# Performance work log

Measured on AMD Instinct MI355X. Metric: run time of the kernel, lower is better.

Reference implementation:

```python
import itertools
import jax, jax.numpy as jnp
import numpy as np

# ---- static config (matches init_kwargs) ----
FRAME_H, FRAME_W = 480, 640
RES = 5               # map_resolution (cm/cell)
Z_RES = 5
MAP_SIZE_CM = 4800 // 2   # after global_downscaling
VR = 100              # vision_range
HFOV = 79.0
DU = 1                # du_scale
CAT_THR, EXP_THR, MAP_THR = 5.0, 1.0, 1.0
NSEM = 16
MAX_H = int(360 / Z_RES)    # 72
MIN_H = int(-80 / Z_RES)    # -16
AGENT_H_CM = 0.88 * 100.0
XC = (FRAME_W - 1.0) / 2.0
ZC = (FRAME_H - 1.0) / 2.0
FOCAL = (FRAME_W / 2.0) / np.tan(np.deg2rad(HFOV / 2.0))
VFOV = np.arctan(FRAME_H / 2.0 / FOCAL)
MIN_VISION = AGENT_H_CM / np.tan(VFOV)
SHIFT_X = VR * RES // 2     # shift_loc[0]; rotation angle is 0 -> identity
DEG = 57.29577951308232


def splat_feat_nd(grid_dims, feat, coords):
    # feat: (B,F,N); coords: (B,3,N) in [-1,1]; trilinear scatter-add splat.
    B, Fc, N = feat.shape
    pos_dim, wts_dim = [], []
    for d in range(3):
        g = grid_dims[d]
        pos = coords[:, d, :] * (g / 2.0) + g / 2.0
        pd, wd = [], []
        for ix in (0, 1):
            p = jnp.floor(pos) + ix
            safe = ((p > 0) & (p < g)).astype(feat.dtype)
            wd.append((1.0 - jnp.abs(pos - p)) * safe)
            pd.append(p * safe)
        pos_dim.append(pd)
        wts_dim.append(wd)
    gflat = jnp.zeros((B, Fc, grid_dims[0] * grid_dims[1] * grid_dims[2]), feat.dtype)
    scatter = jax.vmap(lambda g, i, u: g.at[:, i].add(u))
    for ix_d in itertools.product((0, 1), (0, 1), (0, 1)):
        index = jnp.zeros((B, N), feat.dtype)
        wts = jnp.ones((B, N), feat.dtype)
        for d in range(3):
            index = index * grid_dims[d] + pos_dim[d][ix_d[d]]
            wts = wts * wts_dim[d][ix_d[d]]
        upd = feat * wts[:, None, :]
        gflat = jnp.round(scatter(gflat, index.astype(jnp.int32), upd))  # torch rounds after each pass
    return gflat.reshape(B, Fc, grid_dims[0], grid_dims[1], grid_dims[2])


def affine_grid(theta, H, W):
    # torch F.affine_grid, align_corners=False (default)
    xs = (2.0 * jnp.arange(W) + 1.0) / W - 1.0
    ys = (2.0 * jnp.arange(H) + 1.0) / H - 1.0
    X, Y = jnp.meshgrid(xs, ys, indexing='xy')          # (H,W)
    base = jnp.stack([X, Y, jnp.ones_like(X)], -1)      # (H,W,3)
    return jnp.einsum('bij,hwj->bhwi', theta, base)     # (B,H,W,2)


def grid_sample(img, grid):
    # bilinear, zeros padding, align_corners=True (as in forward)
    B, C, H, W = img.shape
    x = (grid[..., 0] + 1.0) * 0.5 * (W - 1)
    y = (grid[..., 1] + 1.0) * 0.5 * (H - 1)
    x0 = jnp.floor(x)
    y0 = jnp.floor(y)

    def gather(ix, iy):
        valid = ((ix >= 0) & (ix <= W - 1) & (iy >= 0) & (iy <= H - 1)).astype(img.dtype)
        ic = jnp.clip(ix, 0, W - 1).astype(jnp.int32)
        jc = jnp.clip(iy, 0, H - 1).astype(jnp.int32)
        v = jax.vmap(lambda im, jj, ii: im[:, jj, ii])(img, jc, ic)  # (B,C,Ho,Wo)
        return v * valid[:, None]

    wx1 = x - x0
    wx0 = 1.0 - wx1
    wy1 = y - y0
    wy0 = 1.0 - wy1
    return (gather(x0, y0) * (wx0 * wy0)[:, None]
            + gather(x0 + 1, y0) * (wx1 * wy0)[:, None]
            + gather(x0, y0 + 1) * (wx0 * wy1)[:, None]
            + gather(x0 + 1, y0 + 1) * (wx1 * wy1)[:, None])


def reference(obs, pose_obs, maps_last, poses_last, agent_heights):
    bs, c, h, w = obs.shape
    depth = obs[:, 3]
    # ---- point cloud from depth (camera frame) ----
    Y = depth[:, ::DU, ::DU]
    gx = jnp.arange(w, dtype=obs.dtype)[::DU]            # pixel x (width)
    gz = jnp.arange(h - 1, -1, -1, dtype=obs.dtype)[::DU]  # flipped pixel z (height)
    X = (gx[None, None, :] - XC) * Y / FOCAL
    Z = (gz[None, :, None] - ZC) * Y / FOCAL
    Z = Z + agent_heights * 100.0   # camera elevation 0 -> rotation is identity
    X = X + SHIFT_X                 # shift_loc angle pi/2 -> rotation is identity
    # ---- normalize to [-1,1] voxel coords ----
    Xc = ((X / RES) - VR // 2.0) / VR * 2.0
    Yc = ((Y / RES) - VR // 2.0) / VR * 2.0
    Zc = ((Z / Z_RES) - (MAX_H + MIN_H) // 2.0) / (MAX_H - MIN_H) * 2.0
    coords = jnp.stack([Xc, Yc, Zc], axis=1).reshape(bs, 3, -1)   # (B,3,N)
    # ---- per-point features: [occupancy=1, avg-pooled semantics] ----
    hs, ws = h // DU, w // DU
    sem = obs[:, 4:].reshape(bs, c - 4, hs, DU, ws, DU).mean(axis=(3, 5))
    feat = jnp.concatenate([jnp.ones((bs, 1, hs * ws), obs.dtype),
                            sem.reshape(bs, c - 4, hs * ws)], axis=1)
    # ---- splat into voxel grid, then height-axis projections ----
    voxels = splat_feat_nd((VR, VR, MAX_H - MIN_H), feat, coords).swapaxes(2, 3)
    min_z = int(35 / Z_RES - MIN_H)               # 23
    max_z = int((AGENT_H_CM + 1) / Z_RES - MIN_H)  # 33
    floor_z = int(-35 / Z_RES - MIN_H)             # 9
    agent_height_proj = voxels[..., min_z:max_z].sum(-1)
    all_height_proj = voxels.sum(-1)
    mv_std = int(MIN_VISION // Z_RES)
    around_floor = voxels[..., :min_z].sum(-1)
    under_floor = (voxels[..., floor_z:min_z].sum(-1) == 0.0).astype(obs.dtype) * around_floor
    # near-field floor heuristic from last depth row
    depth_row = depth[:, -1, :]
    re_depth = jnp.where(depth_row < 3000.0, depth_row, jnp.asarray(MIN_VISION, obs.dtype))
    count = (re_depth - MIN_VISION - 60.0 > 0).sum(axis=1)
    mask = count > (w / 4.0)
    c1, c2 = (VR - 6) // 2, (VR + 6) // 2
    patch = under_floor[:, 0, mv_std, c1:c2]
    under_floor = under_floor.at[:, 0, mv_std, c1:c2].set(jnp.where(mask[:, None], 1.0, patch))
    fp_map_pred = jnp.clip((agent_height_proj[:, 0:1] + under_floor[:, 0:1]) / MAP_THR, 0.0, 1.0)
    fp_exp_pred = jnp.clip(all_height_proj[:, 0:1] / EXP_THR, 0.0, 1.0)
    # ---- paste into egocentric local map frame ----
    M = MAP_SIZE_CM // RES   # 480
    x1 = M // 2 - VR // 2
    x2 = x1 + VR
    y1 = M // 2
    y2 = y1 + VR
    agent_view = jnp.zeros((bs, c, M, M), obs.dtype)
    agent_view = agent_view.at[:, 0:1, y1:y2, x1:x2].set(fp_map_pred)
    agent_view = agent_view.at[:, 1:2, y1:y2, x1:x2].set(fp_exp_pred)
    agent_view = agent_view.at[:, 4:, y1:y2, x1:x2].set(
        jnp.clip(agent_height_proj[:, 1:] / CAT_THR, 0.0, 1.0))
    # ---- dead-reckoning pose update ----
    th = poses_last[:, 2] / DEG
    ny = poses_last[:, 1] + pose_obs[:, 0] * jnp.sin(th) + pose_obs[:, 1] * jnp.cos(th)
    nx = poses_last[:, 0] + pose_obs[:, 0] * jnp.cos(th) - pose_obs[:, 1] * jnp.sin(th)
    nt = poses_last[:, 2] + pose_obs[:, 2] * DEG
    nt = jnp.fmod(nt - 180.0, 360.0) + 180.0
    nt = jnp.fmod(nt + 180.0, 360.0) - 180.0
    current_poses = jnp.stack([nx, ny, nt], axis=1)
    # ---- spatial transform (rotate then translate) into allocentric map ----
    half = M // 2
    stx = -(nx * 100.0 / RES - half) / half
    sty = -(ny * 100.0 / RES - half) / half
    t = (90.0 - nt) * np.pi / 180.0
    cos_t, sin_t = jnp.cos(t), jnp.sin(t)
    zeros, ones = jnp.zeros_like(cos_t), jnp.ones_like(cos_t)
    theta1 = jnp.stack([jnp.stack([cos_t, -sin_t, zeros], 1),
                        jnp.stack([sin_t, cos_t, zeros], 1)], 1)
    theta2 = jnp.stack([jnp.stack([ones, zeros, stx], 1),
                        jnp.stack([zeros, ones, sty], 1)], 1)
    rotated = grid_sample(agent_view, affine_grid(theta1, M, M))
    translated = grid_sample(rotated, affine_grid(theta2, M, M))
    map_pred = jnp.maximum(maps_last, translated)
    # pose_pred aliases the in-place-updated poses_last in torch == current_poses
    return fp_map_pred, map_pred, current_poses, current_poses


def setup_inputs():
    key = jax.random.key(0)
    k1, k2, k3, k4, k5, k6 = jax.random.split(key, 6)
    bs, c, h, w = 8, 4 + NSEM, FRAME_H, FRAME_W
    obs = jax.random.uniform(k1, (bs, c, h, w), jnp.float32)            # RGB/sem in [0,1]
    depth = jax.random.uniform(k2, (bs, h, w), jnp.float32) * 480.0 + 20.0  # cm
    obs = obs.at[:, 3].set(depth)
    pose_obs = jax.random.normal(k3, (bs, 3), jnp.float32) * jnp.array([0.1, 0.1, 0.05], jnp.float32)
    maps_last = jax.random.uniform(k4, (bs, c, 480, 480), jnp.float32)
    xy = jax.random.uniform(k5, (bs, 2), jnp.float32) * 4.0 + 10.0      # meters, near map center
    ang = jax.random.uniform(k6, (bs, 1), jnp.float32) * 360.0 - 180.0
    poses_last = jnp.concatenate([xy, ang], axis=1)
    agent_heights = jnp.full((bs, 1, 1), 0.88, jnp.float32)
    return {"obs": obs, "pose_obs": pose_obs, "maps_last": maps_last,
            "poses_last": poses_last, "agent_heights": agent_heights}
```

## Files before the change

kernel.cpp:

```cpp
#include <hip/hip_runtime.h>
#include <math.h>

#pragma clang fp contract(off)

#define BS 8
#define CCH 20
#define IMH 480
#define IMW 640
#define HW (IMH*IMW)
#define VRX 100
#define NZ 88
#define NSEMC 16
#define CROP0 124
#define CROPN 232
#define NROTC 18
#define NBINS 880000
#define NBINS2 80000
#define SEMCAP 890000u

__global__ void posemask_kernel(const float* __restrict__ pose_obs,
                                const float* __restrict__ poses_last,
                                const float* __restrict__ obs,
                                float* __restrict__ outp1, float* __restrict__ outp2,
                                float* __restrict__ posebuf, float MINVF) {
#pragma clang fp contract(off)
  int b = blockIdx.x;
  int t = threadIdx.x;
  if (t == 0) {
    const float DEGF = (float)57.29577951308232;
    float th = poses_last[b*3+2] / DEGF;
    float sn = sinf(th), cs = cosf(th);
    float ny = poses_last[b*3+1] + pose_obs[b*3+0]*sn + pose_obs[b*3+1]*cs;
    float nx = poses_last[b*3+0] + pose_obs[b*3+0]*cs - pose_obs[b*3+1]*sn;
    float nt = poses_last[b*3+2] + pose_obs[b*3+2]*DEGF;
    nt = fmodf(nt - 180.0f, 360.0f) + 180.0f;
    nt = fmodf(nt + 180.0f, 360.0f) - 180.0f;
    outp1[b*3+0] = nx; outp1[b*3+1] = ny; outp1[b*3+2] = nt;
    outp2[b*3+0] = nx; outp2[b*3+1] = ny; outp2[b*3+2] = nt;
    float tt = (90.0f - nt) * (float)M_PI / 180.0f;
    float* pb = posebuf + b*8;
    pb[0] = cosf(tt);
    pb[1] = sinf(tt);
    pb[2] = -((nx*100.0f/5.0f - 240.0f)/240.0f);
    pb[3] = -((ny*100.0f/5.0f - 240.0f)/240.0f);
  }
  const float* row = obs + (size_t)b*CCH*HW + 3*(size_t)HW + 479*IMW;
  int cnt = 0;
  for (int col = t; col < IMW; col += 256) {
    float d = row[col];
    float re = (d < 3000.0f) ? d : MINVF;
    float v = re - MINVF;
    v = v - 60.0f;
    if (v > 0.0f) cnt++;
  }
  __shared__ int sh[256];
  sh[t] = cnt;
  __syncthreads();
  for (int s = 128; s > 0; s >>= 1) {
    if (t < s) sh[t] += sh[t + s];
    __syncthreads();
  }
  if (t == 0) posebuf[b*8+4] = (sh[0] > 160) ? 1.0f : 0.0f;
}

__device__ __forceinline__ void transform_pix(int r, int col, float Yd, float ah100,
                                              float FOCALF,
                                              float& pos0, float& pos1, float& pos2) {
#pragma clang fp contract(off)
  float X = ((float)col - 319.5f) * Yd / FOCALF;
  X = X + 250.0f;
  float Z = ((float)(479 - r) - 239.5f) * Yd / FOCALF;
  Z = Z + ah100;
  float Xc = (X/5.0f - 50.0f)/100.0f*2.0f;
  float Yc = (Yd/5.0f - 50.0f)/100.0f*2.0f;
  float Zc = (Z/5.0f - 28.0f)/88.0f*2.0f;
  pos0 = Xc*50.0f + 50.0f;
  pos1 = Yc*50.0f + 50.0f;
  pos2 = Zc*44.0f + 44.0f;
}

__device__ __forceinline__ int bin_key(int b, float pos0, float pos1, float pos2) {
  float f0 = floorf(pos0), f1 = floorf(pos1), f2 = floorf(pos2);
  if (!(f0 >= 0.0f && f0 <= 99.0f && f1 >= 0.0f && f1 <= 99.0f &&
        f2 >= 0.0f && f2 <= 87.0f)) return -1;
  int xi = (int)f0, yi = (int)f1, zi = (int)f2;
  return ((b*100 + yi)*100 + xi)*11 + (zi >> 3);
}

__global__ void bin_count_kernel(const float* __restrict__ obs,
                                 const float* __restrict__ agent_h,
                                 unsigned* __restrict__ cnt, unsigned* __restrict__ cnt2,
                                 float FOCALF) {
#pragma clang fp contract(off)
  int tid = blockIdx.x*256 + threadIdx.x;
#pragma unroll
  for (int u = 0; u < 4; u++) {
    int p = tid + u*614400;
    int b = p / HW;
    int pix = p - b*HW;
    int r = pix / IMW, col = pix - r*IMW;
    float Yd = obs[(size_t)b*CCH*HW + 3*(size_t)HW + pix];
    float ah100 = agent_h[b]*100.0f;
    float pos0, pos1, pos2;
    transform_pix(r, col, Yd, ah100, FOCALF, pos0, pos1, pos2);
    int key = bin_key(b, pos0, pos1, pos2);
    if (key >= 0) {
      atomicAdd(&cnt[key], 1u);
      int zi = (int)floorf(pos2);
      if (zi >= 22 && zi <= 32) atomicAdd(&cnt2[key/11], 1u);
    }
  }
}

__device__ __forceinline__ void scan1_body(const unsigned* __restrict__ cnt,
                                           unsigned* __restrict__ offs,
                                           unsigned* __restrict__ bsum,
                                           int n, int blk, unsigned* sh) {
  int t = threadIdx.x;
  int base = blk*1024 + t*4;
  unsigned v[4];
  unsigned s = 0;
#pragma unroll
  for (int i = 0; i < 4; i++) {
    unsigned c = (base + i < n) ? cnt[base + i] : 0u;
    v[i] = s; s += c;
  }
  sh[t] = s;
  __syncthreads();
  for (int off = 1; off < 256; off <<= 1) {
    unsigned add = (t >= off) ? sh[t - off] : 0u;
    __syncthreads();
    sh[t] += add;
    __syncthreads();
  }
  unsigned texcl = sh[t] - s;
#pragma unroll
  for (int i = 0; i < 4; i++)
    if (base + i < n) offs[base + i] = texcl + v[i];
  if (t == 255) bsum[blk] = sh[255];
}

__global__ void scan1m_kernel(const unsigned* __restrict__ cnt, unsigned* __restrict__ offs,
                              unsigned* __restrict__ bsum,
                              const unsigned* __restrict__ cnt2, unsigned* __restrict__ offs2,
                              unsigned* __restrict__ bsum2) {
  __shared__ unsigned sh[256];
  int blk = blockIdx.x;
  if (blk < 860) scan1_body(cnt, offs, bsum, NBINS, blk, sh);
  else           scan1_body(cnt2, offs2, bsum2, NBINS2, blk - 860, sh);
}

__global__ void scan2m_kernel(unsigned* __restrict__ bsum, unsigned* __restrict__ bsum2) {
  __shared__ unsigned sh[1024];
  unsigned* arr = (blockIdx.x == 0) ? bsum : bsum2;
  int nb = (blockIdx.x == 0) ? 860 : 79;
  int t = threadIdx.x;
  unsigned v = (t < nb) ? arr[t] : 0u;
  sh[t] = v;
  __syncthreads();
  for (int off = 1; off < 1024; off <<= 1) {
    unsigned add = (t >= off) ? sh[t - off] : 0u;
    __syncthreads();
    sh[t] += add;
    __syncthreads();
  }
  if (t < nb) arr[t] = sh[t] - v;
}

__global__ void scan3m_kernel(unsigned* __restrict__ offs, const unsigned* __restrict__ bsum,
                              unsigned* __restrict__ cursor,
                              unsigned* __restrict__ offs2, const unsigned* __restrict__ bsum2,
                              unsigned* __restrict__ cursor2) {
  int blk = blockIdx.x;
  if (blk < 3438) {
    int i = blk*256 + threadIdx.x;
    if (i >= NBINS) return;
    unsigned o = offs[i] + bsum[i >> 10];
    offs[i] = o;
    cursor[i] = o;
  } else {
    int i = (blk - 3438)*256 + threadIdx.x;
    if (i >= NBINS2) return;
    unsigned o = offs2[i] + bsum2[i >> 10];
    offs2[i] = o;
    cursor2[i] = o;
  }
}

__global__ void place_kernel(const float* __restrict__ obs,
                             const float* __restrict__ agent_h,
                             unsigned* __restrict__ cursor,
                             float4* __restrict__ records, float FOCALF) {
#pragma clang fp contract(off)
  int tid = blockIdx.x*256 + threadIdx.x;
#pragma unroll
  for (int u = 0; u < 2; u++) {
    int p = tid + u*1228800;
    int b = p / HW;
    int pix = p - b*HW;
    int r = pix / IMW, col = pix - r*IMW;
    float Yd = obs[(size_t)b*CCH*HW + 3*(size_t)HW + pix];
    float ah100 = agent_h[b]*100.0f;
    float pos0, pos1, pos2;
    transform_pix(r, col, Yd, ah100, FOCALF, pos0, pos1, pos2);
    int key = bin_key(b, pos0, pos1, pos2);
    if (key >= 0) {
      unsigned idx = atomicAdd(&cursor[key], 1u);
      float4 rec;
      rec.x = pos0; rec.y = pos1; rec.z = pos2; rec.w = 0.0f;
      records[idx] = rec;
    }
  }
}

__global__ void __launch_bounds__(256) gatherS_cm_kernel(
    const float4* __restrict__ records, const unsigned* __restrict__ offs,
    const unsigned* __restrict__ cursor, float* __restrict__ colbuf) {
#pragma clang fp contract(off)
  __shared__ float S[256*9];
  __shared__ float red[32][8][4];
  int t = threadIdx.x;
  int k = t & 7, cw = t >> 3;
  int iz = k & 1, ix = (k >> 1) & 1, iy = (k >> 2) & 1;
  int col = blockIdx.x*32 + cw;
  int cx = col % 100, cy = (col/100) % 100;
  bool cellvalid = (cx+ix >= 1) && (cx+ix <= 99) && (cy+iy >= 1) && (cy+iy <= 99);
  float fx = (float)ix, fy = (float)iy, fz = (float)iz;
  float* Sl = &S[t*9];
#pragma unroll
  for (int i = 0; i < 8; i++) Sl[i] = 0.0f;
  float pall = 0.f, pahp = 0.f, par = 0.f, pmid = 0.f;
  int colkey = col*11;
  for (int oct = 0; oct < 11; oct++) {
    unsigned s = offs[colkey + oct], e = cursor[colkey + oct];
    for (unsigned ri = s; ri < e; ri++) {
      float4 rec = records[ri];
      float f0 = floorf(rec.x), f1 = floorf(rec.y), f2 = floorf(rec.z);
      float wx = 1.0f - fabsf(rec.x - (f0 + fx));
      float wy = 1.0f - fabsf(rec.y - (f1 + fy));
      float wz = 1.0f - fabsf(rec.z - (f2 + fz));
      float w = wx*wy;
      w = w*wz;
      int z8 = ((int)f2) & 7;
      Sl[z8] += w;
    }
    int zbase = oct*8;
#pragma unroll
    for (int z8 = 0; z8 < 8; z8++) {
      float a = Sl[z8];
      Sl[z8] = 0.0f;
      int tz = zbase + z8 + iz;
      if (a != 0.0f && tz >= 1 && tz <= 87) {
        float rv = rintf(a);
        pall += rv;
        if (tz < 23) { par += rv; if (tz >= 9) pmid += rv; }
        else if (tz < 33) pahp += rv;
      }
    }
  }
  if (!cellvalid) { pall = 0.f; pahp = 0.f; par = 0.f; pmid = 0.f; }
  red[cw][k][0] = pall;
  red[cw][k][1] = pahp;
  red[cw][k][2] = par;
  red[cw][k][3] = pmid;
  __syncthreads();
  for (int e2 = t; e2 < 512; e2 += 256) {
    int cw2 = e2 >> 4, rem = e2 & 15, c = rem >> 2, p = rem & 3;
    int colw = blockIdx.x*32 + cw2;
    colbuf[colw*16 + rem] = red[cw2][2*c][p] + red[cw2][2*c + 1][p];
  }
}

__global__ void combine_kernel(const float* __restrict__ colbuf,
                               const float* __restrict__ posebuf,
                               float* __restrict__ out0, float* __restrict__ fpexp) {
#pragma clang fp contract(off)
  int tid = blockIdx.x*256 + threadIdx.x;
  if (tid >= 80000) return;
  int b = tid / 10000;
  int yx = tid - b*10000;
  int ty = yx / 100, tx = yx - (yx/100)*100;
  float all = 0.f, ahp = 0.f, ar = 0.f, mid = 0.f;
#pragma unroll
  for (int c = 0; c < 4; c++) {
    int iy = c >> 1, ix = c & 1;
    int cy = ty - iy, cx = tx - ix;
    if (cy < 0 || cx < 0) continue;
    const float* cb = &colbuf[((b*10000 + cy*100 + cx)*4 + c)*4];
    all += cb[0]; ahp += cb[1]; ar += cb[2]; mid += cb[3];
  }
  float u = (mid == 0.0f) ? ar : 0.0f;
  if (ty == 28 && tx >= 47 && tx < 53) {
    if (posebuf[b*8+4] != 0.0f) u = 1.0f;
  }
  float fm = ahp + u;
  out0[tid] = fminf(fmaxf(fm, 0.0f), 1.0f);
  fpexp[tid] = fminf(fmaxf(all, 0.0f), 1.0f);
}

__global__ void semplace_kernel(const float* __restrict__ obs,
                                const float* __restrict__ agent_h,
                                unsigned* __restrict__ cursor2,
                                float* __restrict__ semrec, float FOCALF) {
#pragma clang fp contract(off)
  int tid = blockIdx.x*256 + threadIdx.x;
#pragma unroll
  for (int u = 0; u < 2; u++) {
    int p = tid + u*1228800;
    int b = p / HW;
    int pix = p - b*HW;
    int r = pix / IMW, col = pix - r*IMW;
    const float* obsb = obs + (size_t)b*CCH*HW;
    float Yd = obsb[3*(size_t)HW + pix];
    float ah100 = agent_h[b]*100.0f;
    float pos0, pos1, pos2;
    transform_pix(r, col, Yd, ah100, FOCALF, pos0, pos1, pos2);
    float f0 = floorf(pos0), f1 = floorf(pos1), f2 = floorf(pos2);
    if (f0 >= 0.0f && f0 <= 99.0f && f1 >= 0.0f && f1 <= 99.0f &&
        f2 >= 22.0f && f2 <= 32.0f) {
      int colb = (b*100 + (int)f1)*100 + (int)f0;
      unsigned idx = atomicAdd(&cursor2[colb], 1u);
      if (idx < SEMCAP) {
        float* dp = semrec + (size_t)idx*19;
        dp[0] = pos0; dp[1] = pos1; dp[2] = pos2;
#pragma unroll
        for (int ch = 0; ch < NSEMC; ch++)
          dp[3 + ch] = obsb[(size_t)(4 + ch)*HW + pix];
      }
    }
  }
}

__global__ void __launch_bounds__(128) gatherSem3_kernel(
    const float* __restrict__ semrec, const unsigned* __restrict__ offs2,
    const unsigned* __restrict__ cursor2, float* __restrict__ semacc) {
#pragma clang fp contract(off)
  __shared__ float st[128*84];
  int t = threadIdx.x;
  int ch = t & 15;
  int blk = blockIdx.x;
  int b = blk / 1250, cb = blk - b*1250;
  int colb = b*10000 + cb*8 + (t >> 4);
  int cy = (colb/100) % 100, cx = colb % 100;
  float* S = &st[t*84];
#pragma unroll
  for (int i = 0; i < 80; i++) S[i] = 0.0f;
  unsigned s = offs2[colb], e = cursor2[colb];
  for (unsigned ri = s; ri < e; ri++) {
    const float* rp = semrec + (size_t)ri*19;
    float pos0 = rp[0], pos1 = rp[1], pos2 = rp[2];
    float chv = rp[3 + ch];
    float f0 = floorf(pos0), f1 = floorf(pos1), f2 = floorf(pos2);
    int zi = (int)f2;
    float wx0 = 1.0f - fabsf(pos0 - f0);
    float wx1 = 1.0f - fabsf(pos0 - (f0 + 1.0f));
    float wy0 = 1.0f - fabsf(pos1 - f1);
    float wy1 = 1.0f - fabsf(pos1 - (f1 + 1.0f));
    float w00 = wx0*wy0;
    float w01 = wx1*wy0;
    float w10 = wx0*wy1;
    float w11 = wx1*wy1;
    float wza = 1.0f - fabsf(pos2 - f2);
    float wzb = 1.0f - fabsf(pos2 - (f2 + 1.0f));
#pragma unroll
    for (int iz = 0; iz < 2; iz++) {
      int tzr = zi + iz - 23;
      if (tzr < 0 || tzr > 9) continue;
      float wz = (iz == 0) ? wza : wzb;
      int base = tzr*8 + iz*4;
      S[base + 0] += chv*(w00*wz);
      S[base + 1] += chv*(w01*wz);
      S[base + 2] += chv*(w10*wz);
      S[base + 3] += chv*(w11*wz);
    }
  }
  float s00 = 0.f, s01 = 0.f, s10 = 0.f, s11 = 0.f;
#pragma unroll
  for (int q = 0; q < 20; q++) {
    s00 += rintf(S[q*4 + 0]);
    s01 += rintf(S[q*4 + 1]);
    s10 += rintf(S[q*4 + 2]);
    s11 += rintf(S[q*4 + 3]);
  }
  float* sa = semacc + ((size_t)b*NSEMC + ch)*10000;
  bool vx0 = (cx >= 1), vx1 = (cx <= 98), vy0 = (cy >= 1), vy1 = (cy <= 98);
  if (vy0 && vx0 && s00 != 0.f) atomicAdd(&sa[cy*100 + cx],           s00);
  if (vy0 && vx1 && s01 != 0.f) atomicAdd(&sa[cy*100 + cx + 1],       s01);
  if (vy1 && vx0 && s10 != 0.f) atomicAdd(&sa[(cy + 1)*100 + cx],     s10);
  if (vy1 && vx1 && s11 != 0.f) atomicAdd(&sa[(cy + 1)*100 + cx + 1], s11);
}

__device__ __forceinline__ float fetch_av(const float* __restrict__ out0,
                                          const float* __restrict__ fpexp,
                                          const float* __restrict__ semacc,
                                          int b, int cidx, float xf, float yf) {
  if (!(xf >= 0.0f && xf <= 479.0f && yf >= 0.0f && yf <= 479.0f)) return 0.0f;
  int xi = (int)xf, yi = (int)yf;
  int wx = xi - 190, wy = yi - 240;
  if (wx < 0 || wx >= 100 || wy < 0 || wy >= 100) return 0.0f;
  int o = b*10000 + wy*100 + wx;
  if (cidx == 0) return out0[o];
  if (cidx == 1) return fpexp[o];
  float v = semacc[(size_t)(b*NSEMC + (cidx-2))*10000 + wy*100 + wx] / 5.0f;
  return fminf(fmaxf(v, 0.0f), 1.0f);
}

__global__ void rotate_kernel(const float* __restrict__ out0, const float* __restrict__ fpexp,
                              const float* __restrict__ semacc,
                              const float* __restrict__ posebuf,
                              float* __restrict__ rot) {
#pragma clang fp contract(off)
  int tid = blockIdx.x*256 + threadIdx.x;
  if (tid >= BS*NROTC*CROPN*CROPN) return;
  int cj = tid % CROPN;
  int t1 = tid / CROPN;
  int ci = t1 % CROPN;
  int t2 = t1 / CROPN;
  int cidx = t2 % NROTC;
  int b = t2 / NROTC;
  int i = ci + CROP0, j = cj + CROP0;
  float X = (2.0f*(float)j + 1.0f)/480.0f - 1.0f;
  float Y = (2.0f*(float)i + 1.0f)/480.0f - 1.0f;
  const float* pb = posebuf + b*8;
  float gx = pb[0]*X - pb[1]*Y;
  float gy = pb[1]*X + pb[0]*Y;
  float x = (gx + 1.0f)*0.5f*479.0f;
  float y = (gy + 1.0f)*0.5f*479.0f;
  float x0 = floorf(x), y0 = floorf(y);
  float wx1 = x - x0, wx0 = 1.0f - wx1;
  float wy1 = y - y0, wy0 = 1.0f - wy1;
  float v00 = fetch_av(out0,fpexp,semacc,b,cidx,x0,       y0);
  float v10 = fetch_av(out0,fpexp,semacc,b,cidx,x0+1.0f,  y0);
  float v01 = fetch_av(out0,fpexp,semacc,b,cidx,x0,       y0+1.0f);
  float v11 = fetch_av(out0,fpexp,semacc,b,cidx,x0+1.0f,  y0+1.0f);
  float val = v00*(wx0*wy0) + v10*(wx1*wy0) + v01*(wx0*wy1) + v11*(wx1*wy1);
  rot[tid] = val;
}

__device__ __forceinline__ float fetch_rot(const float* __restrict__ rot,
                                           int b, int cidx, float xf, float yf) {
  if (!(xf >= 0.0f && xf <= 479.0f && yf >= 0.0f && yf <= 479.0f)) return 0.0f;
  int xi = (int)xf, yi = (int)yf;
  int rx = xi - CROP0, ry = yi - CROP0;
  if (rx < 0 || rx >= CROPN || ry < 0 || ry >= CROPN) return 0.0f;
  return rot[((size_t)(b*NROTC + cidx)*CROPN + ry)*CROPN + rx];
}

__global__ void translate_kernel(const float* __restrict__ maps_last,
                                 const float* __restrict__ rot,
                                 const float* __restrict__ posebuf,
                                 float* __restrict__ out1) {
#pragma clang fp contract(off)
  size_t tid = (size_t)blockIdx.x*256 + threadIdx.x;
  if (tid >= (size_t)BS*CCH*480*480) return;
  int j = (int)(tid % 480);
  size_t t1 = tid / 480;
  int i = (int)(t1 % 480);
  size_t t2 = t1 / 480;
  int c = (int)(t2 % CCH);
  int b = (int)(t2 / CCH);
  float ml = maps_last[tid];
  if (c == 2 || c == 3) { out1[tid] = ml; return; }
  int cidx = (c < 2) ? c : c - 2;
  const float* pb = posebuf + b*8;
  float X = (2.0f*(float)j + 1.0f)/480.0f - 1.0f;
  float Y = (2.0f*(float)i + 1.0f)/480.0f - 1.0f;
  float gx = X + pb[2];
  float gy = Y + pb[3];
  float x = (gx + 1.0f)*0.5f*479.0f;
  float y = (gy + 1.0f)*0.5f*479.0f;
  float x0 = floorf(x), y0 = floorf(y);
  float wx1 = x - x0, wx0 = 1.0f - wx1;
  float wy1 = y - y0, wy0 = 1.0f - wy1;
  float v00 = fetch_rot(rot,b,cidx,x0,      y0);
  float v10 = fetch_rot(rot,b,cidx,x0+1.0f, y0);
  float v01 = fetch_rot(rot,b,cidx,x0,      y0+1.0f);
  float v11 = fetch_rot(rot,b,cidx,x0+1.0f, y0+1.0f);
  float val = v00*(wx0*wy0) + v10*(wx1*wy0) + v01*(wx0*wy1) + v11*(wx1*wy1);
  out1[tid] = fmaxf(ml, val);
}

extern "C" void kernel_launch(void* const* d_in, const int* in_sizes, int n_in,
                              void* d_out, int out_size, void* d_ws, size_t ws_size,
                              hipStream_t stream) {
  const float* obs        = (const float*)d_in[0];
  const float* pose_obs   = (const float*)d_in[1];
  const float* maps_last  = (const float*)d_in[2];
  const float* poses_last = (const float*)d_in[3];
  const float* agent_h    = (const float*)d_in[4];
  float* out = (float*)d_out;
  float* ws  = (float*)d_ws;

  const size_t WS_NEED = (size_t)64 + 80000ull + 1280000ull
                       + 880000ull + 80000ull + 880000ull + 880000ull + 1024ull
                       + 80000ull + 80000ull + 1024ull + 16910000ull;
  if (ws_size < WS_NEED*sizeof(float)) return;

  double focal_d = 640.0/2.0/tan(79.0/2.0*M_PI/180.0);
  float FOCALF = (float)focal_d;
  double vfov = atan(480.0/2.0/focal_d);
  float MINVF = (float)((0.88*100.0)/tan(vfov));

  float* posebuf = ws;
  float* fpexp   = ws + 64;
  float* semacc  = fpexp + 80000;
  unsigned* cnt     = (unsigned*)(semacc + 1280000);
  unsigned* cnt2    = cnt + 880000;
  unsigned* offs    = cnt2 + 80000;
  unsigned* cursor  = offs + 880000;
  unsigned* bsum    = cursor + 880000;
  unsigned* offs2   = bsum + 1024;
  unsigned* cursor2 = offs2 + 80000;
  unsigned* bsum2   = cursor2 + 80000;
  float* bigbuf  = (float*)(bsum2 + 1024);
  float4* records = (float4*)bigbuf;
  float* colbuf   = bigbuf + 9830400;
  float* semrec   = bigbuf;
  float* rot      = bigbuf;

  float* out0  = out;
  float* out1  = out + 80000;
  float* outp1 = out1 + (size_t)BS*CCH*480*480;
  float* outp2 = outp1 + 24;

  hipMemsetAsync(semacc, 0, 1280000ull*sizeof(float), stream);
  hipMemsetAsync(cnt, 0, ((size_t)880000 + 80000ull)*sizeof(unsigned), stream);

  posemask_kernel<<<BS, 256, 0, stream>>>(pose_obs, poses_last, obs,
                                          outp1, outp2, posebuf, MINVF);
  bin_count_kernel<<<2400, 256, 0, stream>>>(obs, agent_h, cnt, cnt2, FOCALF);
  scan1m_kernel<<<939, 256, 0, stream>>>(cnt, offs, bsum, cnt2, offs2, bsum2);
  scan2m_kernel<<<2, 1024, 0, stream>>>(bsum, bsum2);
  scan3m_kernel<<<3751, 256, 0, stream>>>(offs, bsum, cursor, offs2, bsum2, cursor2);

  place_kernel<<<4800, 256, 0, stream>>>(obs, agent_h, cursor, records, FOCALF);
  gatherS_cm_kernel<<<2500, 256, 0, stream>>>(records, offs, cursor, colbuf);
  combine_kernel<<<313, 256, 0, stream>>>(colbuf, posebuf, out0, fpexp);

  semplace_kernel<<<4800, 256, 0, stream>>>(obs, agent_h, cursor2, semrec, FOCALF);
  gatherSem3_kernel<<<10000, 128, 0, stream>>>(semrec, offs2, cursor2, semacc);

  rotate_kernel<<<30276, 256, 0, stream>>>(out0, fpexp, semacc, posebuf, rot);
  translate_kernel<<<144000, 256, 0, stream>>>(maps_last, rot, posebuf, out1);
}
```

Before: 824.6 us.

## Fuse semantic placement into place kernel, store pixel indices, vectorize translate

Folds semplace_kernel into place_kernel, so the depth transform and bin test run once per pixel and both record streams are written in a single pass. Records now hold only the pixel index (4 bytes instead of a float4, and 17 floats instead of 19 for semantic records), and the gather kernels recompute positions from depth. This trades extra arithmetic and a dependent depth load for less record traffic. The translate kernel is also vectorized to handle four output pixels per thread with float4 loads and stores.

Result: slower. 996.4 us (+20.8%).

```diff
diff --git a/kernel.cpp b/kernel.cpp
--- a/kernel.cpp
+++ b/kernel.cpp
@@ -16,7 +16,7 @@
 #define NROTC 18
 #define NBINS 880000
 #define NBINS2 80000
-#define SEMCAP 890000u
+#define SEMCAP 780000u
 
 __global__ void posemask_kernel(const float* __restrict__ pose_obs,
                                 const float* __restrict__ poses_last,
@@ -79,14 +79,6 @@
   pos2 = Zc*44.0f + 44.0f;
 }
 
-__device__ __forceinline__ int bin_key(int b, float pos0, float pos1, float pos2) {
-  float f0 = floorf(pos0), f1 = floorf(pos1), f2 = floorf(pos2);
-  if (!(f0 >= 0.0f && f0 <= 99.0f && f1 >= 0.0f && f1 <= 99.0f &&
-        f2 >= 0.0f && f2 <= 87.0f)) return -1;
-  int xi = (int)f0, yi = (int)f1, zi = (int)f2;
-  return ((b*100 + yi)*100 + xi)*11 + (zi >> 3);
-}
-
 __global__ void bin_count_kernel(const float* __restrict__ obs,
                                  const float* __restrict__ agent_h,
                                  unsigned* __restrict__ cnt, unsigned* __restrict__ cnt2,
@@ -103,11 +95,13 @@
     float ah100 = agent_h[b]*100.0f;
     float pos0, pos1, pos2;
     transform_pix(r, col, Yd, ah100, FOCALF, pos0, pos1, pos2);
-    int key = bin_key(b, pos0, pos1, pos2);
-    if (key >= 0) {
-      atomicAdd(&cnt[key], 1u);
-      int zi = (int)floorf(pos2);
-      if (zi >= 22 && zi <= 32) atomicAdd(&cnt2[key/11], 1u);
+    float f0 = floorf(pos0), f1 = floorf(pos1), f2 = floorf(pos2);
+    if (f0 >= 0.0f && f0 <= 99.0f && f1 >= 0.0f && f1 <= 99.0f &&
+        f2 >= 0.0f && f2 <= 87.0f) {
+      int xi = (int)f0, yi = (int)f1, zi = (int)f2;
+      int cb = (b*100 + yi)*100 + xi;
+      atomicAdd(&cnt[cb*11 + (zi >> 3)], 1u);
+      if (zi >= 22 && zi <= 32) atomicAdd(&cnt2[cb], 1u);
     }
   }
 }
@@ -189,8 +183,9 @@
 
 __global__ void place_kernel(const float* __restrict__ obs,
                              const float* __restrict__ agent_h,
-                             unsigned* __restrict__ cursor,
-                             float4* __restrict__ records, float FOCALF) {
+                             unsigned* __restrict__ cursor, unsigned* __restrict__ cursor2,
+                             unsigned* __restrict__ recs, float* __restrict__ semrec,
+                             float FOCALF) {
 #pragma clang fp contract(off)
   int tid = blockIdx.x*256 + threadIdx.x;
 #pragma unroll
@@ -198,24 +193,38 @@
     int p = tid + u*1228800;
     int b = p / HW;
     int pix = p - b*HW;
-    int r = pix / IMW, col = pix - r*IMW;
-    float Yd = obs[(size_t)b*CCH*HW + 3*(size_t)HW + pix];
+    int r = pix / IMW, c = pix - r*IMW;
+    const float* obsb = obs + (size_t)b*CCH*HW;
+    float Yd = obsb[3*(size_t)HW + pix];
     float ah100 = agent_h[b]*100.0f;
     float pos0, pos1, pos2;
-    transform_pix(r, col, Yd, ah100, FOCALF, pos0, pos1, pos2);
-    int key = bin_key(b, pos0, pos1, pos2);
-    if (key >= 0) {
-      unsigned idx = atomicAdd(&cursor[key], 1u);
-      float4 rec;
-      rec.x = pos0; rec.y = pos1; rec.z = pos2; rec.w = 0.0f;
-      records[idx] = rec;
+    transform_pix(r, c, Yd, ah100, FOCALF, pos0, pos1, pos2);
+    float f0 = floorf(pos0), f1 = floorf(pos1), f2 = floorf(pos2);
+    if (f0 >= 0.0f && f0 <= 99.0f && f1 >= 0.0f && f1 <= 99.0f &&
+        f2 >= 0.0f && f2 <= 87.0f) {
+      int xi = (int)f0, yi = (int)f1, zi = (int)f2;
+      int cb = (b*100 + yi)*100 + xi;
+      unsigned idx = atomicAdd(&cursor[cb*11 + (zi >> 3)], 1u);
+      recs[idx] = (unsigned)pix;
+      if (zi >= 22 && zi <= 32) {
+        unsigned i2 = atomicAdd(&cursor2[cb], 1u);
+        if (i2 < SEMCAP) {
+          float* sp = semrec + (size_t)i2*17;
+          sp[0] = __uint_as_float((unsigned)pix);
+#pragma unroll
+          for (int ch = 0; ch < NSEMC; ch++)
+            sp[1 + ch] = obsb[(size_t)(4 + ch)*HW + pix];
+        }
+      }
     }
   }
 }
 
 __global__ void __launch_bounds__(256) gatherS_cm_kernel(
-    const float4* __restrict__ records, const unsigned* __restrict__ offs,
-    const unsigned* __restrict__ cursor, float* __restrict__ colbuf) {
+    const unsigned* __restrict__ recs, const unsigned* __restrict__ offs,
+    const unsigned* __restrict__ cursor,
+    const float* __restrict__ obs, const float* __restrict__ agent_h,
+    float* __restrict__ colbuf, float FOCALF) {
 #pragma clang fp contract(off)
   __shared__ float S[256*9];
   __shared__ float red[32][8][4];
@@ -223,7 +232,10 @@
   int k = t & 7, cw = t >> 3;
   int iz = k & 1, ix = (k >> 1) & 1, iy = (k >> 2) & 1;
   int col = blockIdx.x*32 + cw;
+  int b = col / 10000;
   int cx = col % 100, cy = (col/100) % 100;
+  const float* depthb = obs + (size_t)b*CCH*HW + 3*(size_t)HW;
+  float ah100 = agent_h[b]*100.0f;
   bool cellvalid = (cx+ix >= 1) && (cx+ix <= 99) && (cy+iy >= 1) && (cy+iy <= 99);
   float fx = (float)ix, fy = (float)iy, fz = (float)iz;
   float* Sl = &S[t*9];
@@ -234,11 +246,15 @@
   for (int oct = 0; oct < 11; oct++) {
     unsigned s = offs[colkey + oct], e = cursor[colkey + oct];
     for (unsigned ri = s; ri < e; ri++) {
-      float4 rec = records[ri];
-      float f0 = floorf(rec.x), f1 = floorf(rec.y), f2 = floorf(rec.z);
-      float wx = 1.0f - fabsf(rec.x - (f0 + fx));
-      float wy = 1.0f - fabsf(rec.y - (f1 + fy));
-      float wz = 1.0f - fabsf(rec.z - (f2 + fz));
+      unsigned pix = recs[ri];
+      int rr = pix / IMW, cc = pix - rr*IMW;
+      float Yd = depthb[pix];
+      float pos0, pos1, pos2;
+      transform_pix(rr, cc, Yd, ah100, FOCALF, pos0, pos1, pos2);
+      float f0 = floorf(pos0), f1 = floorf(pos1), f2 = floorf(pos2);
+      float wx = 1.0f - fabsf(pos0 - (f0 + fx));
+      float wy = 1.0f - fabsf(pos1 - (f1 + fy));
+      float wz = 1.0f - fabsf(pos2 - (f2 + fz));
       float w = wx*wy;
       w = w*wz;
       int z8 = ((int)f2) & 7;
@@ -298,42 +314,11 @@
   fpexp[tid] = fminf(fmaxf(all, 0.0f), 1.0f);
 }
 
-__global__ void semplace_kernel(const float* __restrict__ obs,
-                                const float* __restrict__ agent_h,
-                                unsigned* __restrict__ cursor2,
-                                float* __restrict__ semrec, float FOCALF) {
-#pragma clang fp contract(off)
-  int tid = blockIdx.x*256 + threadIdx.x;
-#pragma unroll
-  for (int u = 0; u < 2; u++) {
-    int p = tid + u*1228800;
-    int b = p / HW;
-    int pix = p - b*HW;
-    int r = pix / IMW, col = pix - r*IMW;
-    const float* obsb = obs + (size_t)b*CCH*HW;
-    float Yd = obsb[3*(size_t)HW + pix];
-    float ah100 = agent_h[b]*100.0f;
-    float pos0, pos1, pos2;
-    transform_pix(r, col, Yd, ah100, FOCALF, pos0, pos1, pos2);
-    float f0 = floorf(pos0), f1 = floorf(pos1), f2 = floorf(pos2);
-    if (f0 >= 0.0f && f0 <= 99.0f && f1 >= 0.0f && f1 <= 99.0f &&
-        f2 >= 22.0f && f2 <= 32.0f) {
-      int colb = (b*100 + (int)f1)*100 + (int)f0;
-      unsigned idx = atomicAdd(&cursor2[colb], 1u);
-      if (idx < SEMCAP) {
-        float* dp = semrec + (size_t)idx*19;
-        dp[0] = pos0; dp[1] = pos1; dp[2] = pos2;
-#pragma unroll
-        for (int ch = 0; ch < NSEMC; ch++)
-          dp[3 + ch] = obsb[(size_t)(4 + ch)*HW + pix];
-      }
-    }
-  }
-}
-
 __global__ void __launch_bounds__(128) gatherSem3_kernel(
     const float* __restrict__ semrec, const unsigned* __restrict__ offs2,
-    const unsigned* __restrict__ cursor2, float* __restrict__ semacc) {
+    const unsigned* __restrict__ cursor2,
+    const float* __restrict__ obs, const float* __restrict__ agent_h,
+    float* __restrict__ semacc, float FOCALF) {
 #pragma clang fp contract(off)
   __shared__ float st[128*84];
   int t = threadIdx.x;
@@ -342,14 +327,20 @@
   int b = blk / 1250, cb = blk - b*1250;
   int colb = b*10000 + cb*8 + (t >> 4);
   int cy = (colb/100) % 100, cx = colb % 100;
+  const float* depthb = obs + (size_t)b*CCH*HW + 3*(size_t)HW;
+  float ah100 = agent_h[b]*100.0f;
   float* S = &st[t*84];
 #pragma unroll
   for (int i = 0; i < 80; i++) S[i] = 0.0f;
   unsigned s = offs2[colb], e = cursor2[colb];
   for (unsigned ri = s; ri < e; ri++) {
-    const float* rp = semrec + (size_t)ri*19;
-    float pos0 = rp[0], pos1 = rp[1], pos2 = rp[2];
-    float chv = rp[3 + ch];
+    const float* rp = semrec + (size_t)ri*17;
+    unsigned pix = __float_as_uint(rp[0]);
+    float chv = rp[1 + ch];
+    int rr = pix / IMW, cc = pix - rr*IMW;
+    float Yd = depthb[pix];
+    float pos0, pos1, pos2;
+    transform_pix(rr, cc, Yd, ah100, FOCALF, pos0, pos1, pos2);
     float f0 = floorf(pos0), f1 = floorf(pos1), f2 = floorf(pos2);
     int zi = (int)f2;
     float wx0 = 1.0f - fabsf(pos0 - f0);
@@ -451,33 +442,42 @@
                                  const float* __restrict__ posebuf,
                                  float* __restrict__ out1) {
 #pragma clang fp contract(off)
-  size_t tid = (size_t)blockIdx.x*256 + threadIdx.x;
-  if (tid >= (size_t)BS*CCH*480*480) return;
-  int j = (int)(tid % 480);
-  size_t t1 = tid / 480;
-  int i = (int)(t1 % 480);
-  size_t t2 = t1 / 480;
-  int c = (int)(t2 % CCH);
-  int b = (int)(t2 / CCH);
-  float ml = maps_last[tid];
-  if (c == 2 || c == 3) { out1[tid] = ml; return; }
+  int tid = blockIdx.x*256 + threadIdx.x;
+  if (tid >= 9216000) return;
+  int q = tid % 120;
+  int t1 = tid / 120;
+  int i = t1 % 480;
+  int t2 = t1 / 480;
+  int c = t2 % CCH;
+  int b = t2 / CCH;
+  size_t base = (size_t)tid * 4;
+  float4 ml = *(const float4*)&maps_last[base];
+  if (c == 2 || c == 3) { *(float4*)&out1[base] = ml; return; }
   int cidx = (c < 2) ? c : c - 2;
   const float* pb = posebuf + b*8;
-  float X = (2.0f*(float)j + 1.0f)/480.0f - 1.0f;
   float Y = (2.0f*(float)i + 1.0f)/480.0f - 1.0f;
-  float gx = X + pb[2];
   float gy = Y + pb[3];
-  float x = (gx + 1.0f)*0.5f*479.0f;
   float y = (gy + 1.0f)*0.5f*479.0f;
-  float x0 = floorf(x), y0 = floorf(y);
-  float wx1 = x - x0, wx0 = 1.0f - wx1;
+  float y0 = floorf(y);
   float wy1 = y - y0, wy0 = 1.0f - wy1;
-  float v00 = fetch_rot(rot,b,cidx,x0,      y0);
-  float v10 = fetch_rot(rot,b,cidx,x0+1.0f, y0);
-  float v01 = fetch_rot(rot,b,cidx,x0,      y0+1.0f);
-  float v11 = fetch_rot(rot,b,cidx,x0+1.0f, y0+1.0f);
-  float val = v00*(wx0*wy0) + v10*(wx1*wy0) + v01*(wx0*wy1) + v11*(wx1*wy1);
-  out1[tid] = fmaxf(ml, val);
+  float res[4];
+  const float* mlp = (const float*)&ml;
+#pragma unroll
+  for (int e = 0; e < 4; e++) {
+    int j = q*4 + e;
+    float X = (2.0f*(float)j + 1.0f)/480.0f - 1.0f;
+    float gx = X + pb[2];
+    float x = (gx + 1.0f)*0.5f*479.0f;
+    float x0 = floorf(x);
+    float wx1 = x - x0, wx0 = 1.0f - wx1;
+    float v00 = fetch_rot(rot,b,cidx,x0,      y0);
+    float v10 = fetch_rot(rot,b,cidx,x0+1.0f, y0);
+    float v01 = fetch_rot(rot,b,cidx,x0,      y0+1.0f);
+    float v11 = fetch_rot(rot,b,cidx,x0+1.0f, y0+1.0f);
+    float val = v00*(wx0*wy0) + v10*(wx1*wy0) + v01*(wx0*wy1) + v11*(wx1*wy1);
+    res[e] = fmaxf(mlp[e], val);
+  }
+  *(float4*)&out1[base] = make_float4(res[0], res[1], res[2], res[3]);
 }
 
 extern "C" void kernel_launch(void* const* d_in, const int* in_sizes, int n_in,
@@ -493,7 +493,8 @@
 
   const size_t WS_NEED = (size_t)64 + 80000ull + 1280000ull
                        + 880000ull + 80000ull + 880000ull + 880000ull + 1024ull
-                       + 80000ull + 80000ull + 1024ull + 16910000ull;
+                       + 80000ull + 80000ull + 1024ull
+                       + 2457600ull + 13260000ull + 1280000ull;
   if (ws_size < WS_NEED*sizeof(float)) return;
 
   double focal_d = 640.0/2.0/tan(79.0/2.0*M_PI/180.0);
@@ -513,9 +514,9 @@
   unsigned* cursor2 = offs2 + 80000;
   unsigned* bsum2   = cursor2 + 80000;
   float* bigbuf  = (float*)(bsum2 + 1024);
-  float4* records = (float4*)bigbuf;
-  float* colbuf   = bigbuf + 9830400;
-  float* semrec   = bigbuf;
+  unsigned* recs  = (unsigned*)bigbuf;
+  float* semrec   = bigbuf + 2457600;
+  float* colbuf   = semrec + 13260000;
   float* rot      = bigbuf;
 
   float* out0  = out;
@@ -533,13 +534,14 @@
   scan2m_kernel<<<2, 1024, 0, stream>>>(bsum, bsum2);
   scan3m_kernel<<<3751, 256, 0, stream>>>(offs, bsum, cursor, offs2, bsum2, cursor2);
 
-  place_kernel<<<4800, 256, 0, stream>>>(obs, agent_h, cursor, records, FOCALF);
-  gatherS_cm_kernel<<<2500, 256, 0, stream>>>(records, offs, cursor, colbuf);
+  place_kernel<<<4800, 256, 0, stream>>>(obs, agent_h, cursor, cursor2,
+                                         recs, semrec, FOCALF);
+  gatherS_cm_kernel<<<2500, 256, 0, stream>>>(recs, offs, cursor, obs, agent_h,
+                                              colbuf, FOCALF);
   combine_kernel<<<313, 256, 0, stream>>>(colbuf, posebuf, out0, fpexp);
-
-  semplace_kernel<<<4800, 256, 0, stream>>>(obs, agent_h, cursor2, semrec, FOCALF);
-  gatherSem3_kernel<<<10000, 128, 0, stream>>>(semrec, offs2, cursor2, semacc);
+  gatherSem3_kernel<<<10000, 128, 0, stream>>>(semrec, offs2, cursor2, obs, agent_h,
+                                               semacc, FOCALF);
 
   rotate_kernel<<<30276, 256, 0, stream>>>(out0, fpexp, semacc, posebuf, rot);
-  translate_kernel<<<144000, 256, 0, stream>>>(maps_last, rot, posebuf, out1);
-}
+  translate_kernel<<<36000, 256, 0, stream>>>(maps_last, rot, posebuf, out1);
+}
```
